# Kernel tuning notes

Measured on AMD Instinct MI355X. Metric: run time of the kernel, lower is better.

Reference implementation:

```python
import jax, jax.numpy as jnp
import numpy as np


def setup_inputs() -> dict:
    key = jax.random.key(0)
    img = jax.random.uniform(key, (3, 4096, 4096), dtype=jnp.float32)
    return {"img": img, "param": 500}


def reference(img, param):
    # Original: poissonNoise = np.random.poisson(param, img.shape).astype(float)
    #           noisy = img + poissonNoise
    noise_key = jax.random.fold_in(jax.random.key(0), 1)
    noise = jax.random.poisson(noise_key, float(param), shape=img.shape).astype(img.dtype)
    return img + noise
```

## Files before the change

### kernel.cpp

```cpp
#include <hip/hip_runtime.h>
#include <stdint.h>
#include <math.h>


#pragma clang fp contract(off)

#define TOTAL_ELEMS 50331648u
#define N_BLOCKS    2048
#define N_TPB       256
#define TOTAL_THREADS 524288u
#define ELEMS_PER_THREAD 96
#define CAP 32
#define TAB_LO 256
#define TAB_N  512
#define QCAP 3072
#define LOG_LAM ((float)6.2146080984221914)

__device__ __forceinline__ uint32_t rotl32(uint32_t v, uint32_t r) {
  return (v << r) | (v >> (32u - r));
}

__device__ __forceinline__ void tf2x32(uint32_t k0, uint32_t k1,
                                       uint32_t c0, uint32_t c1,
                                       uint32_t& o0, uint32_t& o1) {
  uint32_t ks2 = k0 ^ k1 ^ 0x1BD11BDAu;
  uint32_t x0 = c0 + k0;
  uint32_t x1 = c1 + k1;
#define TF_R(r) { x0 += x1; x1 = rotl32(x1, r); x1 ^= x0; }
  TF_R(13u) TF_R(15u) TF_R(26u) TF_R(6u)
  x0 += k1;  x1 += ks2 + 1u;
  TF_R(17u) TF_R(29u) TF_R(16u) TF_R(24u)
  x0 += ks2; x1 += k0 + 2u;
  TF_R(13u) TF_R(15u) TF_R(26u) TF_R(6u)
  x0 += k0;  x1 += k1 + 3u;
  TF_R(17u) TF_R(29u) TF_R(16u) TF_R(24u)
  x0 += k1;  x1 += ks2 + 4u;
  TF_R(13u) TF_R(15u) TF_R(26u) TF_R(6u)
  x0 += ks2; x1 += k0 + 5u;
#undef TF_R
  o0 = x0; o1 = x1;
}

__device__ __forceinline__ float xla_logf(float xin) {
  #pragma clang fp contract(off)
  if (xin == 0.0f) return -__builtin_inff();
  if (!(xin > 0.0f)) return __builtin_nanf("");
  float x = fmaxf(xin, __uint_as_float(0x00800000u));
  uint32_t ix = __float_as_uint(x);
  float e = 1.0f + (float)((int32_t)(ix >> 23) - 127);
  x = __uint_as_float((ix & 0x807fffffu) | 0x3f000000u);
  const float SQRTHF = (float)0.707106781186547524;
  bool m = x < SQRTHF;
  float tmp1 = m ? x : 0.0f;
  x = x - 1.0f;
  e = e - (m ? 1.0f : 0.0f);
  x = x + tmp1;
  float x2 = x * x;
  float x3 = x2 * x;
  float y  = __builtin_fmaf(x, (float)7.0376836292e-2,  (float)-1.1514610310e-1);
  float y1 = __builtin_fmaf(x, (float)-1.2420140846e-1, (float)1.4249322787e-1);
  float y2 = __builtin_fmaf(x, (float)2.0000714765e-1,  (float)-2.4999993993e-1);
  y  = __builtin_fmaf(y,  x, (float)1.1676998740e-1);
  y1 = __builtin_fmaf(y1, x, (float)-1.6668057665e-1);
  y2 = __builtin_fmaf(y2, x, (float)3.3333331174e-1);
  y  = __builtin_fmaf(y, x3, y1);
  y  = __builtin_fmaf(y, x3, y2);
  float yq1 = (float)-2.12194440e-4 * e;
  y = __builtin_fmaf(y, x3, yq1);
  x = __builtin_fmaf(-0.5f, x2, x);
  x = x + y;
  x = __builtin_fmaf((float)0.693359375, e, x);
  return x;
}

__device__ __forceinline__ float xla_log1pf(float x) {
  #pragma clang fp contract(off)
  float for_small = __builtin_fmaf(-0.5f, x, 1.0f) * x;
  float for_large = xla_logf(x + 1.0f);
  return (fabsf(x) < (float)1e-4) ? for_small : for_large;
}

__device__ __forceinline__ float xla_lgammaf(float a) {
  #pragma clang fp contract(off)
  float z = a - 1.0f;
  float sum = (float)0.99999999999980993227684700473478;
  sum = sum + (float)676.520368121885098567009190444019   / (z + 1.0f);
  sum = sum + (float)-1259.13921672240287047156078755283  / (z + 2.0f);
  sum = sum + (float)771.3234287776530788486528258894     / (z + 3.0f);
  sum = sum + (float)-176.61502916214059906584551354      / (z + 4.0f);
  sum = sum + (float)12.507343278686904814458936853       / (z + 5.0f);
  sum = sum + (float)-0.13857109526572011689554707        / (z + 6.0f);
  sum = sum + (float)9.984369578019570859563e-6           / (z + 7.0f);
  sum = sum + (float)1.50563273514931155834e-7            / (z + 8.0f);
  float t = (float)7.5 + z;
  float w = z * (float)(1.0 / 7.5);
  float log_t = (float)2.0149030205422647 + xla_log1pf(w);
  float factor = (z + 0.5f) - t / log_t;
  float log_y = __builtin_fmaf(factor, log_t, (float)0.91893853320467274178)
                + xla_logf(sum);
  return log_y;
}

__device__ __forceinline__ float t_of_k(float k) {
  #pragma clang fp contract(off)
  return __builtin_fmaf(k, LOG_LAM, -500.0f) - xla_lgammaf(k + 1.0f);
}

struct PC { float bb, aa, twoa, inv_alpha, v_r; };

__device__ __forceinline__ PC make_pc() {
  #pragma clang fp contract(off)
  PC c;
  float sq = (float)22.360679774997896;
  c.bb = (float)0.931 + (float)2.53 * sq;
  c.aa = (float)-0.059 + (float)0.02483 * c.bb;
  c.twoa = 2.0f * c.aa;
  c.inv_alpha = (float)1.1239 + (float)1.1328 / (c.bb - (float)3.4);
  c.v_r = (float)0.9277 - (float)3.6224 / (c.bb - 2.0f);
  return c;
}

__device__ __forceinline__ float bits_to_u01(uint32_t bits) {
  return __uint_as_float((bits >> 9) | 0x3f800000u) - 1.0f;
}

__device__ __forceinline__ bool hormann_accept(uint32_t ubits, uint32_t vbits,
                                               const PC& c, const float* __restrict__ ttab,
                                               float& kout) {
  #pragma clang fp contract(off)
  float u01 = bits_to_u01(ubits);
  float v   = bits_to_u01(vbits);
  float u = u01 - 0.5f;
  float us = 0.5f - fabsf(u);
  float inner = c.twoa / us + c.bb;
  float kq = __builtin_fmaf(inner, u, 500.43f);
  float k = floorf(kq);
  kout = k;
  bool accept1 = (us >= (float)0.07) & (v <= c.v_r);
  if (accept1) return true;
  bool reject = (k < 0.0f) | ((us < (float)0.013) & (v > us));
  if (reject) return false;
  float s = xla_logf((v * c.inv_alpha) / (c.aa / (us * us) + c.bb));
  int ki = (int)k;
  float t;
  if (ki >= TAB_LO && ki < TAB_LO + TAB_N) t = ttab[ki - TAB_LO];
  else t = t_of_k(k);
  return s <= t;
}

__device__ __forceinline__ uint32_t pbits(uint32_t s0, uint32_t s1, uint32_t e) {
  uint32_t a, b;
  tf2x32(s0, s1, 0u, e, a, b);
  return a ^ b;
}

__device__ __forceinline__ bool trial(uint32_t e, uint32_t tlvl,
                                      const uint32_t (&ssub)[CAP][4],
                                      const PC& c, const float* __restrict__ ttab,
                                      float& kout) {
  uint32_t ub = pbits(ssub[tlvl][0], ssub[tlvl][1], e);
  uint32_t vb = pbits(ssub[tlvl][2], ssub[tlvl][3], e);
  return hormann_accept(ub, vb, c, ttab, kout);
}

__device__ __forceinline__ void build_shared(uint32_t n, uint32_t (&ssub)[CAP][4],
                                             float* ttab) {
  for (uint32_t i = threadIdx.x; i < TAB_N; i += N_TPB) {
    ttab[i] = t_of_k((float)(int)(TAB_LO + (int)i));
  }
  if (threadIdx.x == 0) {
    uint32_t k0, k1;
    tf2x32(0u, 0u, 0u, 1u, k0, k1);
    for (uint32_t t = 0; t < n; ++t) {
      uint32_t nk0, nk1, s00, s01, s10, s11;
      tf2x32(k0, k1, 0u, 0u, nk0, nk1);
      tf2x32(k0, k1, 0u, 1u, s00, s01);
      tf2x32(k0, k1, 0u, 2u, s10, s11);
      ssub[t][0] = s00; ssub[t][1] = s01;
      ssub[t][2] = s10; ssub[t][3] = s11;
      k0 = nk0; k1 = nk1;
    }
  }
  __syncthreads();
}

__global__ void pn_init(uint32_t* nmax) { *nmax = 0u; }

__global__ __launch_bounds__(N_TPB) void pn_pass1(uint32_t* nmax) {
  __shared__ uint32_t ssub[CAP][4];
  __shared__ float ttab[TAB_N];
  __shared__ uint32_t q[2][QCAP];
  __shared__ uint32_t qn[2];
  __shared__ uint32_t shN;
  if (threadIdx.x == 0) { qn[0] = 0; qn[1] = 0; shN = 1; }
  build_shared(CAP, ssub, ttab);
  PC c = make_pc();
  uint32_t tid_g = blockIdx.x * N_TPB + threadIdx.x;
  for (int j = 0; j < ELEMS_PER_THREAD; ++j) {
    uint32_t e = tid_g + (uint32_t)j * TOTAL_THREADS;
    float kk;
    if (!trial(e, 0u, ssub, c, ttab, kk)) {
      uint32_t idx = atomicAdd(&qn[0], 1u);
      if (__builtin_expect(idx < QCAP, 1)) q[0][idx] = e;
      else {
        uint32_t Lc = CAP;
        for (uint32_t t2 = 1; t2 < CAP; ++t2) {
          if (trial(e, t2, ssub, c, ttab, kk)) { Lc = t2 + 1u; break; }
        }
        atomicMax(&shN, Lc);
      }
    }
  }
  __syncthreads();
  int cur = 0;
  uint32_t localN = 1;
  for (uint32_t t = 1; t < CAP; ++t) {
    uint32_t n = qn[cur]; if (n > QCAP) n = QCAP;
    if (n == 0) break;
    localN = t + 1u;
    if (threadIdx.x == 0) qn[cur ^ 1] = 0;
    __syncthreads();
    for (uint32_t i = threadIdx.x; i < n; i += N_TPB) {
      uint32_t e = q[cur][i];
      float kk;
      if (!trial(e, t, ssub, c, ttab, kk)) {
        uint32_t idx = atomicAdd(&qn[cur ^ 1], 1u);
        if (__builtin_expect(idx < QCAP, 1)) q[cur ^ 1][idx] = e;
        else {
          uint32_t Lc = CAP;
          for (uint32_t t2 = t + 1; t2 < CAP; ++t2) {
            if (trial(e, t2, ssub, c, ttab, kk)) { Lc = t2 + 1u; break; }
          }
          atomicMax(&shN, Lc);
        }
      }
    }
    __syncthreads();
    cur ^= 1;
  }
  __syncthreads();
  if (threadIdx.x == 0) {
    uint32_t m = shN; if (localN > m) m = localN;
    atomicMax(nmax, m);
  }
}

__global__ __launch_bounds__(N_TPB) void pn_pass2(const float* __restrict__ img,
                                                  float* __restrict__ out,
                                                  const uint32_t* __restrict__ nptr) {
  __shared__ uint32_t ssub[CAP][4];
  __shared__ float ttab[TAB_N];
  __shared__ uint32_t q[2][QCAP];
  __shared__ uint32_t qn[2];
  uint32_t N = *nptr;
  if (N < 1u) N = 1u;
  if (N > CAP) N = CAP;
  if (threadIdx.x == 0) { qn[0] = 0; qn[1] = 0; }
  build_shared(N, ssub, ttab);
  PC c = make_pc();
  uint32_t tid_g = blockIdx.x * N_TPB + threadIdx.x;
  uint32_t top = N - 1u;
  for (int j = 0; j < ELEMS_PER_THREAD; ++j) {
    uint32_t e = tid_g + (uint32_t)j * TOTAL_THREADS;
    float kk;
    if (trial(e, top, ssub, c, ttab, kk)) {
      out[e] = img[e] + kk;
    } else {
      uint32_t idx = atomicAdd(&qn[0], 1u);
      if (__builtin_expect(idx < QCAP, 1)) q[0][idx] = e;
      else {
        float kf = -1.0f;
        for (int t2 = (int)top - 1; t2 >= 0; --t2) {
          if (trial(e, (uint32_t)t2, ssub, c, ttab, kk)) { kf = kk; break; }
        }
        out[e] = img[e] + kf;
      }
    }
  }
  __syncthreads();
  int cur = 0;
  for (int t = (int)top - 1; t >= 0; --t) {
    uint32_t n = qn[cur]; if (n > QCAP) n = QCAP;
    if (n == 0) break;
    if (threadIdx.x == 0) qn[cur ^ 1] = 0;
    __syncthreads();
    for (uint32_t i = threadIdx.x; i < n; i += N_TPB) {
      uint32_t e = q[cur][i];
      float kk;
      if (trial(e, (uint32_t)t, ssub, c, ttab, kk)) {
        out[e] = img[e] + kk;
      } else {
        uint32_t idx = atomicAdd(&qn[cur ^ 1], 1u);
        if (__builtin_expect(idx < QCAP, 1)) q[cur ^ 1][idx] = e;
        else {
          float kf = -1.0f;
          for (int t2 = t - 1; t2 >= 0; --t2) {
            if (trial(e, (uint32_t)t2, ssub, c, ttab, kk)) { kf = kk; break; }
          }
          out[e] = img[e] + kf;
        }
      }
    }
    __syncthreads();
    cur ^= 1;
  }
  uint32_t n = qn[cur]; if (n > QCAP) n = QCAP;
  for (uint32_t i = threadIdx.x; i < n; i += N_TPB) {
    uint32_t e = q[cur][i];
    out[e] = img[e] - 1.0f;
  }
}

extern "C" void kernel_launch(void* const* d_in, const int* in_sizes, int n_in,
                              void* d_out, int out_size, void* d_ws, size_t ws_size,
                              hipStream_t stream) {
  (void)in_sizes; (void)n_in; (void)out_size; (void)ws_size;
  const float* img = (const float*)d_in[0];
  float* out = (float*)d_out;
  uint32_t* nmax = (uint32_t*)d_ws;
  pn_init<<<1, 1, 0, stream>>>(nmax);
  pn_pass1<<<N_BLOCKS, N_TPB, 0, stream>>>(nmax);
  pn_pass2<<<N_BLOCKS, N_TPB, 0, stream>>>(img, out, nmax);
}
```

Before: 821.2 us.

## Compact slow-path Hormann acceptance into shared queues with wave-aggregated pushes

The first-trial loop now processes elements in chunks. Elements that miss the fast acceptance test are compacted into a shared-memory queue, and the expensive log/table test then runs on dense warps, which is meant to cut divergence in the hot loop. Queue pushes switch to ballot-based wave-aggregated atomics, and queue entries shrink to 16-bit local indices. In exchange there are extra __syncthreads per chunk, more shared memory (which may lower occupancy), and duplicated overflow fallback paths.

```diff
diff --git a/kernel.cpp b/kernel.cpp
--- a/kernel.cpp
+++ b/kernel.cpp
@@ -14,6 +14,8 @@
 #define TAB_LO 256
 #define TAB_N  512
 #define QCAP 3072
+#define CHUNK_J 4
+#define AQ_CAP 384
 #define LOG_LAM ((float)6.2146080984221914)
 
 __device__ __forceinline__ uint32_t rotl32(uint32_t v, uint32_t r) {
@@ -124,6 +126,12 @@
   return __uint_as_float((bits >> 9) | 0x3f800000u) - 1.0f;
 }
 
+__device__ __forceinline__ float t_lookup(float k, const float* __restrict__ ttab) {
+  int ki = (int)k;
+  if (ki >= TAB_LO && ki < TAB_LO + TAB_N) return ttab[ki - TAB_LO];
+  return t_of_k(k);
+}
+
 __device__ __forceinline__ bool hormann_accept(uint32_t ubits, uint32_t vbits,
                                                const PC& c, const float* __restrict__ ttab,
                                                float& kout) {
@@ -141,11 +149,7 @@
   bool reject = (k < 0.0f) | ((us < (float)0.013) & (v > us));
   if (reject) return false;
   float s = xla_logf((v * c.inv_alpha) / (c.aa / (us * us) + c.bb));
-  int ki = (int)k;
-  float t;
-  if (ki >= TAB_LO && ki < TAB_LO + TAB_N) t = ttab[ki - TAB_LO];
-  else t = t_of_k(k);
-  return s <= t;
+  return s <= t_lookup(k, ttab);
 }
 
 __device__ __forceinline__ uint32_t pbits(uint32_t s0, uint32_t s1, uint32_t e) {
@@ -161,6 +165,22 @@
   uint32_t ub = pbits(ssub[tlvl][0], ssub[tlvl][1], e);
   uint32_t vb = pbits(ssub[tlvl][2], ssub[tlvl][3], e);
   return hormann_accept(ub, vb, c, ttab, kout);
+}
+
+__device__ __forceinline__ uint32_t lane_id() {
+  return __builtin_amdgcn_mbcnt_hi(~0u, __builtin_amdgcn_mbcnt_lo(~0u, 0u));
+}
+
+__device__ __forceinline__ uint32_t wq_push(uint32_t* counter, bool push) {
+  uint64_t mask = __ballot(push);
+  if (mask == 0ull) return 0xFFFFFFFFu;
+  uint32_t lane = lane_id();
+  int leader = (int)(__ffsll((unsigned long long)mask) - 1);
+  uint32_t base = 0;
+  if ((int)lane == leader) base = atomicAdd(counter, (uint32_t)__popcll(mask));
+  base = (uint32_t)__shfl((int)base, leader);
+  uint32_t off = (uint32_t)__popcll(mask & ((1ull << lane) - 1ull));
+  return base + off;
 }
 
 __device__ __forceinline__ void build_shared(uint32_t n, uint32_t (&ssub)[CAP][4],
@@ -189,29 +209,86 @@
 __global__ __launch_bounds__(N_TPB) void pn_pass1(uint32_t* nmax) {
   __shared__ uint32_t ssub[CAP][4];
   __shared__ float ttab[TAB_N];
-  __shared__ uint32_t q[2][QCAP];
+  __shared__ uint16_t qf[2][QCAP];
   __shared__ uint32_t qn[2];
   __shared__ uint32_t shN;
+  __shared__ uint16_t aq_li[AQ_CAP];
+  __shared__ float aq_u[AQ_CAP];
+  __shared__ float aq_v[AQ_CAP];
+  __shared__ uint32_t aqn;
   if (threadIdx.x == 0) { qn[0] = 0; qn[1] = 0; shN = 1; }
   build_shared(CAP, ssub, ttab);
   PC c = make_pc();
-  uint32_t tid_g = blockIdx.x * N_TPB + threadIdx.x;
-  for (int j = 0; j < ELEMS_PER_THREAD; ++j) {
-    uint32_t e = tid_g + (uint32_t)j * TOTAL_THREADS;
-    float kk;
-    if (!trial(e, 0u, ssub, c, ttab, kk)) {
-      uint32_t idx = atomicAdd(&qn[0], 1u);
-      if (__builtin_expect(idx < QCAP, 1)) q[0][idx] = e;
-      else {
-        uint32_t Lc = CAP;
-        for (uint32_t t2 = 1; t2 < CAP; ++t2) {
-          if (trial(e, t2, ssub, c, ttab, kk)) { Lc = t2 + 1u; break; }
-        }
-        atomicMax(&shN, Lc);
-      }
-    }
-  }
-  __syncthreads();
+  uint32_t blockBase = blockIdx.x * N_TPB;
+  for (int jc = 0; jc < ELEMS_PER_THREAD; jc += CHUNK_J) {
+    if (threadIdx.x == 0) aqn = 0;
+    __syncthreads();
+    for (int j = jc; j < jc + CHUNK_J; ++j) {
+      uint32_t e = blockBase + threadIdx.x + (uint32_t)j * TOTAL_THREADS;
+      uint16_t li = (uint16_t)(((uint32_t)j << 8) | threadIdx.x);
+      uint32_t ub = pbits(ssub[0][0], ssub[0][1], e);
+      uint32_t vb = pbits(ssub[0][2], ssub[0][3], e);
+      float u01 = bits_to_u01(ub);
+      float v   = bits_to_u01(vb);
+      float u = u01 - 0.5f;
+      float us = 0.5f - fabsf(u);
+      bool accept1 = (us >= (float)0.07) & (v <= c.v_r);
+      bool pend = !accept1;
+      uint32_t ai = wq_push(&aqn, pend);
+      if (pend) {
+        if (__builtin_expect(ai < AQ_CAP, 1)) {
+          aq_li[ai] = li; aq_u[ai] = u; aq_v[ai] = v;
+        } else {
+          float inner = c.twoa / us + c.bb;
+          float k = floorf(__builtin_fmaf(inner, u, 500.43f));
+          bool reject = (k < 0.0f) | ((us < (float)0.013) & (v > us));
+          bool acc = false;
+          if (!reject) {
+            float s = xla_logf((v * c.inv_alpha) / (c.aa / (us * us) + c.bb));
+            acc = (s <= t_lookup(k, ttab));
+          }
+          if (!acc) {
+            uint32_t qi = atomicAdd(&qn[0], 1u);
+            if (qi < QCAP) qf[0][qi] = li;
+            else {
+              float kk; uint32_t Lc = CAP;
+              for (uint32_t t2 = 1; t2 < CAP; ++t2)
+                if (trial(e, t2, ssub, c, ttab, kk)) { Lc = t2 + 1u; break; }
+              atomicMax(&shN, Lc);
+            }
+          }
+        }
+      }
+    }
+    __syncthreads();
+    uint32_t an = aqn; if (an > AQ_CAP) an = AQ_CAP;
+    for (uint32_t i = threadIdx.x; i < an; i += N_TPB) {
+      uint16_t li = aq_li[i];
+      float u = aq_u[i], v = aq_v[i];
+      float us = 0.5f - fabsf(u);
+      float inner = c.twoa / us + c.bb;
+      float k = floorf(__builtin_fmaf(inner, u, 500.43f));
+      bool reject = (k < 0.0f) | ((us < (float)0.013) & (v > us));
+      bool acc = false;
+      if (!reject) {
+        float s = xla_logf((v * c.inv_alpha) / (c.aa / (us * us) + c.bb));
+        acc = (s <= t_lookup(k, ttab));
+      }
+      bool fail = !acc;
+      uint32_t qi = wq_push(&qn[0], fail);
+      if (fail) {
+        if (__builtin_expect(qi < QCAP, 1)) qf[0][qi] = li;
+        else {
+          uint32_t e = blockBase + (li & 255u) + (uint32_t)(li >> 8) * TOTAL_THREADS;
+          float kk; uint32_t Lc = CAP;
+          for (uint32_t t2 = 1; t2 < CAP; ++t2)
+            if (trial(e, t2, ssub, c, ttab, kk)) { Lc = t2 + 1u; break; }
+          atomicMax(&shN, Lc);
+        }
+      }
+    }
+    __syncthreads();
+  }
   int cur = 0;
   uint32_t localN = 1;
   for (uint32_t t = 1; t < CAP; ++t) {
@@ -221,16 +298,17 @@
     if (threadIdx.x == 0) qn[cur ^ 1] = 0;
     __syncthreads();
     for (uint32_t i = threadIdx.x; i < n; i += N_TPB) {
-      uint32_t e = q[cur][i];
+      uint16_t li = qf[cur][i];
+      uint32_t e = blockBase + (li & 255u) + (uint32_t)(li >> 8) * TOTAL_THREADS;
       float kk;
-      if (!trial(e, t, ssub, c, ttab, kk)) {
-        uint32_t idx = atomicAdd(&qn[cur ^ 1], 1u);
-        if (__builtin_expect(idx < QCAP, 1)) q[cur ^ 1][idx] = e;
+      bool fail = !trial(e, t, ssub, c, ttab, kk);
+      uint32_t qi = wq_push(&qn[cur ^ 1], fail);
+      if (fail) {
+        if (__builtin_expect(qi < QCAP, 1)) qf[cur ^ 1][qi] = li;
         else {
           uint32_t Lc = CAP;
-          for (uint32_t t2 = t + 1; t2 < CAP; ++t2) {
+          for (uint32_t t2 = t + 1; t2 < CAP; ++t2)
             if (trial(e, t2, ssub, c, ttab, kk)) { Lc = t2 + 1u; break; }
-          }
           atomicMax(&shN, Lc);
         }
       }
@@ -250,34 +328,91 @@
                                                   const uint32_t* __restrict__ nptr) {
   __shared__ uint32_t ssub[CAP][4];
   __shared__ float ttab[TAB_N];
-  __shared__ uint32_t q[2][QCAP];
+  __shared__ uint16_t qf[2][QCAP];
   __shared__ uint32_t qn[2];
+  __shared__ uint16_t aq_li[AQ_CAP];
+  __shared__ float aq_k[AQ_CAP];
+  __shared__ float aq_us[AQ_CAP];
+  __shared__ float aq_v[AQ_CAP];
+  __shared__ uint32_t aqn;
   uint32_t N = *nptr;
   if (N < 1u) N = 1u;
   if (N > CAP) N = CAP;
   if (threadIdx.x == 0) { qn[0] = 0; qn[1] = 0; }
   build_shared(N, ssub, ttab);
   PC c = make_pc();
-  uint32_t tid_g = blockIdx.x * N_TPB + threadIdx.x;
+  uint32_t blockBase = blockIdx.x * N_TPB;
   uint32_t top = N - 1u;
-  for (int j = 0; j < ELEMS_PER_THREAD; ++j) {
-    uint32_t e = tid_g + (uint32_t)j * TOTAL_THREADS;
-    float kk;
-    if (trial(e, top, ssub, c, ttab, kk)) {
-      out[e] = img[e] + kk;
-    } else {
-      uint32_t idx = atomicAdd(&qn[0], 1u);
-      if (__builtin_expect(idx < QCAP, 1)) q[0][idx] = e;
-      else {
-        float kf = -1.0f;
-        for (int t2 = (int)top - 1; t2 >= 0; --t2) {
-          if (trial(e, (uint32_t)t2, ssub, c, ttab, kk)) { kf = kk; break; }
-        }
-        out[e] = img[e] + kf;
-      }
-    }
-  }
-  __syncthreads();
+  for (int jc = 0; jc < ELEMS_PER_THREAD; jc += CHUNK_J) {
+    if (threadIdx.x == 0) aqn = 0;
+    __syncthreads();
+    for (int j = jc; j < jc + CHUNK_J; ++j) {
+      uint32_t e = blockBase + threadIdx.x + (uint32_t)j * TOTAL_THREADS;
+      uint16_t li = (uint16_t)(((uint32_t)j << 8) | threadIdx.x);
+      uint32_t ub = pbits(ssub[top][0], ssub[top][1], e);
+      uint32_t vb = pbits(ssub[top][2], ssub[top][3], e);
+      float u01 = bits_to_u01(ub);
+      float v   = bits_to_u01(vb);
+      float u = u01 - 0.5f;
+      float us = 0.5f - fabsf(u);
+      float inner = c.twoa / us + c.bb;
+      float k = floorf(__builtin_fmaf(inner, u, 500.43f));
+      bool accept1 = (us >= (float)0.07) & (v <= c.v_r);
+      bool reject  = (!accept1) & ((k < 0.0f) | ((us < (float)0.013) & (v > us)));
+      bool need2   = (!accept1) & (!reject);
+      if (accept1) out[e] = img[e] + k;
+      uint32_t qi = wq_push(&qn[0], reject);
+      if (reject) {
+        if (__builtin_expect(qi < QCAP, 1)) qf[0][qi] = li;
+        else {
+          float kk, kf = -1.0f;
+          for (int t2 = (int)top - 1; t2 >= 0; --t2)
+            if (trial(e, (uint32_t)t2, ssub, c, ttab, kk)) { kf = kk; break; }
+          out[e] = img[e] + kf;
+        }
+      }
+      uint32_t ai = wq_push(&aqn, need2);
+      if (need2) {
+        if (__builtin_expect(ai < AQ_CAP, 1)) {
+          aq_li[ai] = li; aq_k[ai] = k; aq_us[ai] = us; aq_v[ai] = v;
+        } else {
+          float s = xla_logf((v * c.inv_alpha) / (c.aa / (us * us) + c.bb));
+          if (s <= t_lookup(k, ttab)) out[e] = img[e] + k;
+          else {
+            uint32_t qi2 = atomicAdd(&qn[0], 1u);
+            if (qi2 < QCAP) qf[0][qi2] = li;
+            else {
+              float kk, kf = -1.0f;
+              for (int t2 = (int)top - 1; t2 >= 0; --t2)
+                if (trial(e, (uint32_t)t2, ssub, c, ttab, kk)) { kf = kk; break; }
+              out[e] = img[e] + kf;
+            }
+          }
+        }
+      }
+    }
+    __syncthreads();
+    uint32_t an = aqn; if (an > AQ_CAP) an = AQ_CAP;
+    for (uint32_t i = threadIdx.x; i < an; i += N_TPB) {
+      uint16_t li = aq_li[i];
+      float k = aq_k[i], us = aq_us[i], v = aq_v[i];
+      uint32_t e = blockBase + (li & 255u) + (uint32_t)(li >> 8) * TOTAL_THREADS;
+      float s = xla_logf((v * c.inv_alpha) / (c.aa / (us * us) + c.bb));
+      bool acc = (s <= t_lookup(k, ttab));
+      if (acc) out[e] = img[e] + k;
+      uint32_t qi = wq_push(&qn[0], !acc);
+      if (!acc) {
+        if (__builtin_expect(qi < QCAP, 1)) qf[0][qi] = li;
+        else {
+          float kk, kf = -1.0f;
+          for (int t2 = (int)top - 1; t2 >= 0; --t2)
+            if (trial(e, (uint32_t)t2, ssub, c, ttab, kk)) { kf = kk; break; }
+          out[e] = img[e] + kf;
+        }
+      }
+    }
+    __syncthreads();
+  }
   int cur = 0;
   for (int t = (int)top - 1; t >= 0; --t) {
     uint32_t n = qn[cur]; if (n > QCAP) n = QCAP;
@@ -285,18 +420,18 @@
     if (threadIdx.x == 0) qn[cur ^ 1] = 0;
     __syncthreads();
     for (uint32_t i = threadIdx.x; i < n; i += N_TPB) {
-      uint32_t e = q[cur][i];
+      uint16_t li = qf[cur][i];
+      uint32_t e = blockBase + (li & 255u) + (uint32_t)(li >> 8) * TOTAL_THREADS;
       float kk;
-      if (trial(e, (uint32_t)t, ssub, c, ttab, kk)) {
-        out[e] = img[e] + kk;
-      } else {
-        uint32_t idx = atomicAdd(&qn[cur ^ 1], 1u);
-        if (__builtin_expect(idx < QCAP, 1)) q[cur ^ 1][idx] = e;
+      bool acc = trial(e, (uint32_t)t, ssub, c, ttab, kk);
+      if (acc) out[e] = img[e] + kk;
+      uint32_t qi = wq_push(&qn[cur ^ 1], !acc);
+      if (!acc) {
+        if (__builtin_expect(qi < QCAP, 1)) qf[cur ^ 1][qi] = li;
         else {
-          float kf = -1.0f;
-          for (int t2 = t - 1; t2 >= 0; --t2) {
-            if (trial(e, (uint32_t)t2, ssub, c, ttab, kk)) { kf = kk; break; }
-          }
+          float kk2, kf = -1.0f;
+          for (int t2 = t - 1; t2 >= 0; --t2)
+            if (trial(e, (uint32_t)t2, ssub, c, ttab, kk2)) { kf = kk2; break; }
           out[e] = img[e] + kf;
         }
       }
@@ -306,7 +441,8 @@
   }
   uint32_t n = qn[cur]; if (n > QCAP) n = QCAP;
   for (uint32_t i = threadIdx.x; i < n; i += N_TPB) {
-    uint32_t e = q[cur][i];
+    uint16_t li = qf[cur][i];
+    uint32_t e = blockBase + (li & 255u) + (uint32_t)(li >> 8) * TOTAL_THREADS;
     out[e] = img[e] - 1.0f;
   }
 }
```

New measurement: 802.5 us. 2.3% less time.
